# Optimization experiments

Measured on AMD Instinct MI355X. Metric: run time of the kernel, lower is better.

Reference implementation:

```python
import jax, jax.numpy as jnp
import numpy as np

B, S, D_IN, D_H, D_LAT, D_OUT = 128, 1024, 64, 256, 256, 128
N_PIECES = 20
NEG_BIG = -99999.0


def setup_inputs() -> dict:
    key = jax.random.key(0)
    ks = jax.random.split(key, 12)
    def lin(k, fan_in, fan_out):
        bound = 1.0 / np.sqrt(fan_in)
        kw, kb = jax.random.split(k)
        w = jax.random.uniform(kw, (fan_in, fan_out), minval=-bound, maxval=bound, dtype=jnp.float32)
        b = jax.random.uniform(kb, (fan_out,), minval=-bound, maxval=bound, dtype=jnp.float32)
        return w, b
    x = jax.random.normal(ks[0], (B, S, D_IN), dtype=jnp.float32)
    mask = jax.random.randint(ks[1], (B, S, 1), 0, 2, dtype=jnp.int32)
    phi_w1, phi_b1 = lin(ks[2], D_IN, D_H)
    phi_w2, phi_b2 = lin(ks[3], D_H, D_LAT)
    rho_w1, rho_b1 = lin(ks[4], D_LAT, D_H)
    rho_w2, rho_b2 = lin(ks[5], D_H, D_OUT)
    pool_w = 0.1 * jax.random.normal(ks[6], (D_LAT, N_PIECES + 1), dtype=jnp.float32)
    return dict(x=x, mask=mask, phi_w1=phi_w1, phi_b1=phi_b1, phi_w2=phi_w2, phi_b2=phi_b2,
                rho_w1=rho_w1, rho_b1=rho_b1, rho_w2=rho_w2, rho_b2=rho_b2, pool_w=pool_w)


def _fspool(x, n, w):
    # x: [B, C, S] features per channel over set dim; n: [B] ragged sizes; w: [C, P+1]
    b, c, s = x.shape
    # positions mapped to [0,1] ratio of the (n-1)-long valid prefix (fill_sizes)
    ratio = jnp.arange(s, dtype=jnp.float32)[None, :] / jnp.maximum(n.astype(jnp.float32) - 1.0, 1.0)[:, None]  # [B,S]
    m = (ratio <= 1.0).astype(x.dtype)          # [B,S], first n positions valid
    ratio = jnp.minimum(ratio, 1.0)
    # piecewise-linear interpolation of continuous weight function (determine_weight)
    pos = N_PIECES * ratio                       # [B,S]
    idx = jnp.floor(pos).astype(jnp.int32)
    frac = (pos - idx)[:, None, :]               # [B,1,S]
    left = jnp.take(w, idx, axis=1).transpose(1, 0, 2)                                   # [B,C,S]
    right = jnp.take(w, jnp.clip(idx + 1, 0, N_PIECES), axis=1).transpose(1, 0, 2)       # [B,C,S]
    weight = (1.0 - frac) * left + frac * right  # [B,C,S]
    # push padded entries to the bottom, sort descending per channel
    xm = x + (1.0 - m)[:, None, :] * NEG_BIG
    xs = jnp.flip(jnp.sort(xm, axis=2), axis=2)  # descending
    return jnp.sum(xs * weight * m[:, None, :], axis=2)  # [B,C]


def reference(x, mask, phi_w1, phi_b1, phi_w2, phi_b2, rho_w1, rho_b1, rho_w2, rho_b2, pool_w):
    # phi per-element MLP: [B,S,d_in] -> [B,S,d_lat]
    h = jax.nn.relu(jnp.einsum('bsi,ih->bsh', x, phi_w1) + phi_b1)
    feat = jnp.einsum('bsh,hl->bsl', h, phi_w2) + phi_b2
    feat = jnp.transpose(feat, (0, 2, 1))        # [B, d_lat, S]
    n = jnp.sum(mask, axis=1).squeeze(-1)        # [B]
    pooled = _fspool(feat, n, pool_w)            # [B, d_lat]
    # rho MLP
    h2 = jax.nn.relu(pooled @ rho_w1 + rho_b1)
    return h2 @ rho_w2 + rho_b2                  # [B, d_out]
```

## Files before the change

kernel.cpp:

```cpp
#include <hip/hip_runtime.h>
#include <hip/hip_bf16.h>

#define B_    128
#define S_    1024
#define DIN   64
#define DH    256
#define DLAT  256
#define DOUT  128
#define NPIECES 20

typedef short bf16x8 __attribute__((ext_vector_type(8)));
typedef float f32x4  __attribute__((ext_vector_type(4)));
typedef unsigned short u16x2 __attribute__((ext_vector_type(2)));

__device__ __forceinline__ unsigned short f2b(float f) {
    union { float f; unsigned u; } a; a.f = f;
    unsigned r = a.u + 0x7fffu + ((a.u >> 16) & 1u);
    return (unsigned short)(r >> 16);
}
__device__ __forceinline__ float b2f_u(unsigned u16bits) {
    union { unsigned u; float f; } a; a.u = u16bits << 16;
    return a.f;
}

__device__ __forceinline__ unsigned pmaxu(unsigned a, unsigned b) {
    union { unsigned u; u16x2 v; } A, Bv, R;
    A.u = a; Bv.u = b;
    R.v = __builtin_elementwise_max(A.v, Bv.v);
    return R.u;
}
__device__ __forceinline__ unsigned pminu(unsigned a, unsigned b) {
    union { unsigned u; u16x2 v; } A, Bv, R;
    A.u = a; Bv.u = b;
    R.v = __builtin_elementwise_min(A.v, Bv.v);
    return R.u;
}

__global__ __launch_bounds__(256) void k_count(const int* __restrict__ mask,
                                               int* __restrict__ nv) {
    int b = blockIdx.x, t = threadIdx.x;
    int sum = 0;
    #pragma unroll
    for (int q = 0; q < S_ / 256; ++q) sum += mask[b * S_ + q * 256 + t];
    #pragma unroll
    for (int off = 32; off > 0; off >>= 1) sum += __shfl_down(sum, off, 64);
    __shared__ int parts[4];
    if ((t & 63) == 0) parts[t >> 6] = sum;
    __syncthreads();
    if (t == 0) {
        int n = parts[0] + parts[1] + parts[2] + parts[3];
        nv[b] = max(n, 2);
    }
}

__global__ __launch_bounds__(256) void k_pack_x(const float* __restrict__ x,
                                                short* __restrict__ xpk) {
    int c = blockIdx.x * 256 + threadIdx.x;
    int l  = c & 63;
    int ks = (c >> 6) & 1;
    int st = (c >> 7) & 63;
    int b  = c >> 13;
    int s  = st * 16 + (l & 15);
    int k0 = ks * 32 + (l >> 4) * 8;
    const float* src = x + ((size_t)(b * S_ + s)) * DIN + k0;
    float4 v0 = *(const float4*)src;
    float4 v1 = *(const float4*)(src + 4);
    bf16x8 o;
    o[0] = (short)f2b(v0.x); o[1] = (short)f2b(v0.y); o[2] = (short)f2b(v0.z); o[3] = (short)f2b(v0.w);
    o[4] = (short)f2b(v1.x); o[5] = (short)f2b(v1.y); o[6] = (short)f2b(v1.z); o[7] = (short)f2b(v1.w);
    *(bf16x8*)(xpk + (size_t)c * 8) = o;
}

__global__ __launch_bounds__(256) void k_pack_w(const float* __restrict__ src,
                                                short* __restrict__ dst,
                                                int KT, int N, int nchunk) {
    int c = blockIdx.x * 256 + threadIdx.x;
    if (c >= nchunk) return;
    int l  = c & 63;
    int ks = (c >> 6) % KT;
    int nt = (c >> 6) / KT;
    int col = nt * 16 + (l & 15);
    int k0  = ks * 32 + (l >> 4) * 8;
    bf16x8 o;
    #pragma unroll
    for (int j = 0; j < 8; ++j) o[j] = (short)f2b(src[(size_t)(k0 + j) * N + col]);
    *(bf16x8*)(dst + (size_t)c * 8) = o;
}

__global__ __launch_bounds__(256) void k_phi_mfma(const short* __restrict__ xpk,
                                                  const short* __restrict__ w1pk,
                                                  const short* __restrict__ w2pk,
                                                  const float* __restrict__ b1,
                                                  const float* __restrict__ b2,
                                                  const int* __restrict__ nv,
                                                  unsigned short* __restrict__ feat) {
    const int b    = blockIdx.y;
    const int tile = blockIdx.x;
    const int s0   = tile * 64;
    if (s0 >= nv[b]) return;
    const int tid  = threadIdx.x;
    const int w    = tid >> 6;
    const int lane = tid & 63;
    const int c15  = lane & 15;
    const int q    = lane >> 4;

    __shared__ __align__(16) char lds[64 * 256 * 2];

    f32x4 acc1[4][4];
    #pragma unroll
    for (int mt = 0; mt < 4; ++mt)
        #pragma unroll
        for (int nt = 0; nt < 4; ++nt) acc1[mt][nt] = (f32x4)0.f;

    const short* xb = xpk + (((size_t)b * 64 + tile * 4) * 2) * 64 * 8;
    bf16x8 a1[4][2], bw[4][2];
    #pragma unroll
    for (int mt = 0; mt < 4; ++mt)
        #pragma unroll
        for (int ks = 0; ks < 2; ++ks)
            a1[mt][ks] = *(const bf16x8*)(xb + ((size_t)(mt * 2 + ks) * 64 + lane) * 8);
    #pragma unroll
    for (int nt = 0; nt < 4; ++nt)
        #pragma unroll
        for (int ks = 0; ks < 2; ++ks)
            bw[nt][ks] = *(const bf16x8*)(w1pk + ((size_t)((w * 4 + nt) * 2 + ks) * 64 + lane) * 8);
    #pragma unroll
    for (int ks = 0; ks < 2; ++ks)
        #pragma unroll
        for (int mt = 0; mt < 4; ++mt)
            #pragma unroll
            for (int nt = 0; nt < 4; ++nt)
                acc1[mt][nt] = __builtin_amdgcn_mfma_f32_16x16x32_bf16(a1[mt][ks], bw[nt][ks], acc1[mt][nt], 0, 0, 0);

    #pragma unroll
    for (int nt = 0; nt < 4; ++nt) {
        int chan = (w * 4 + nt) * 16 + c15;
        float bias = b1[chan];
        #pragma unroll
        for (int mt = 0; mt < 4; ++mt)
            #pragma unroll
            for (int r = 0; r < 4; ++r) {
                int pos = mt * 16 + q * 4 + r;
                float hv = fmaxf(acc1[mt][nt][r] + bias, 0.f);
                int byte = pos * 512 + chan * 2;
                byte ^= (pos & 7) << 4;
                *(unsigned short*)(lds + byte) = f2b(hv);
            }
    }
    __syncthreads();

    f32x4 acc2[4][4];
    #pragma unroll
    for (int mt = 0; mt < 4; ++mt)
        #pragma unroll
        for (int nt = 0; nt < 4; ++nt) acc2[mt][nt] = (f32x4)0.f;

    for (int ks2 = 0; ks2 < 8; ++ks2) {
        bf16x8 af[4];
        #pragma unroll
        for (int mt = 0; mt < 4; ++mt) {
            int pos = mt * 16 + c15;
            int byte = pos * 512 + ks2 * 64 + q * 16;
            byte ^= (pos & 7) << 4;
            af[mt] = *(const bf16x8*)(lds + byte);
        }
        #pragma unroll
        for (int nt = 0; nt < 4; ++nt) {
            bf16x8 bf_ = *(const bf16x8*)(w2pk + ((size_t)((w * 4 + nt) * 8 + ks2) * 64 + lane) * 8);
            #pragma unroll
            for (int mt = 0; mt < 4; ++mt)
                acc2[mt][nt] = __builtin_amdgcn_mfma_f32_16x16x32_bf16(af[mt], bf_, acc2[mt][nt], 0, 0, 0);
        }
    }
    __syncthreads();

    #pragma unroll
    for (int nt = 0; nt < 4; ++nt) {
        int chan = (w * 4 + nt) * 16 + c15;
        float bias = b2[chan];
        #pragma unroll
        for (int mt = 0; mt < 4; ++mt) {
            unsigned u0 = (unsigned)f2b(acc2[mt][nt][0] + bias) | ((unsigned)f2b(acc2[mt][nt][1] + bias) << 16);
            unsigned u1 = (unsigned)f2b(acc2[mt][nt][2] + bias) | ((unsigned)f2b(acc2[mt][nt][3] + bias) << 16);
            int pos0 = mt * 16 + q * 4;
            int byte = chan * 128 + pos0 * 2;
            byte ^= (chan & 7) << 4;
            *(uint2*)(lds + byte) = uint2{u0, u1};
        }
    }
    __syncthreads();

    #pragma unroll
    for (int it = 0; it < 8; ++it) {
        int L = it * 256 + tid;
        int chan = L >> 3, chunk = L & 7;
        int byte = chan * 128 + chunk * 16;
        byte ^= (chan & 7) << 4;
        uint4 val = *(const uint4*)(lds + byte);
        *(uint4*)((char*)(feat + ((size_t)b * DLAT + chan) * S_ + s0) + chunk * 16) = val;
    }
}

template <int EPL, bool FASTW>
__device__ __forceinline__ float fsp_sum(const unsigned short* __restrict__ fp,
                                         int n, const float* __restrict__ pw, int lane) {
    constexpr int NREG = EPL / 2;
    constexpr int N = EPL * 64;
    const int base = lane * EPL;

    unsigned r[NREG];
    {
        const uint4* q = (const uint4*)(fp + base);
        uint4 a = q[0];
        r[0] = a.x; r[1] = a.y; r[2] = a.z; r[3] = a.w;
        if (EPL == 16) {
            uint4 bq = q[1];
            r[4] = bq.x; r[5] = bq.y; r[6] = bq.z; r[7] = bq.w;
        }
    }

    #pragma unroll
    for (int t = 0; t < NREG; ++t) {
        unsigned u = r[t];
        unsigned sgn = (u >> 15) & 0x00010001u;
        unsigned key = u ^ ((sgn * 0x7FFFu) | 0x80008000u);
        int i0 = base + 2 * t;
        unsigned keep = (i0 + 1 < n) ? 0xFFFFFFFFu : ((i0 < n) ? 0x0000FFFFu : 0u);
        r[t] = key & keep;
    }

    #pragma unroll
    for (int k = 2; k <= N; k <<= 1) {
        #pragma unroll
        for (int j = k >> 1; j > 0; j >>= 1) {
            if (j >= EPL) {
                const int m = j / EPL;
                const bool dz  = (((lane * EPL) & k) == 0);
                const bool sel = (dz == ((lane & m) == 0));
                #pragma unroll
                for (int t = 0; t < NREG; ++t) {
                    unsigned p = __shfl_xor(r[t], m, 64);
                    unsigned mx = pmaxu(r[t], p), mn = pminu(r[t], p);
                    r[t] = sel ? mx : mn;
                }
            } else if (j >= 2) {
                const int jr = j >> 1;
                #pragma unroll
                for (int t = 0; t < NREG; ++t) {
                    if ((t & jr) == 0) {
                        const int tb = t | jr;
                        unsigned mx = pmaxu(r[t], r[tb]), mn = pminu(r[t], r[tb]);
                        const bool dz = ((((lane * EPL) | (2 * t)) & k) == 0);
                        r[t]  = dz ? mx : mn;
                        r[tb] = dz ? mn : mx;
                    }
                }
            } else {
                #pragma unroll
                for (int t = 0; t < NREG; ++t) {
                    unsigned sw = (r[t] >> 16) | (r[t] << 16);
                    unsigned mx = pmaxu(r[t], sw), mn = pminu(r[t], sw);
                    const bool dz = ((((lane * EPL) | (2 * t)) & k) == 0);
                    unsigned de = (mx & 0x0000FFFFu) | (mn & 0xFFFF0000u);
                    unsigned as = (mn & 0x0000FFFFu) | (mx & 0xFFFF0000u);
                    r[t] = dz ? de : as;
                }
            }
        }
    }

    const float invd = 1.0f / (float)(n - 1);
    float acc = 0.f;

    float k0, k1, k2; int ib = 0;
    if (FASTW) {
        float rb = fminf((float)base * invd, 1.0f);
        ib = (int)((float)NPIECES * rb);
        if (ib > NPIECES) ib = NPIECES;
        k0 = pw[ib];
        k1 = pw[min(ib + 1, NPIECES)];
        k2 = pw[min(ib + 2, NPIECES)];
    }

    #pragma unroll
    for (int t = 0; t < NREG; ++t) {
        #pragma unroll
        for (int h = 0; h < 2; ++h) {
            int i = base + 2 * t + h;
            unsigned key = h ? (r[t] >> 16) : (r[t] & 0xFFFFu);
            unsigned tneg = ((key >> 15) & 1u) ^ 1u;
            unsigned u = key ^ (0x8000u | (tneg * 0x7FFFu));
            float v = (i < n) ? b2f_u(u) : 0.f;
            float ratio = fminf((float)i * invd, 1.0f);
            float pos = (float)NPIECES * ratio;
            int idx = (int)pos;
            float frac = pos - (float)idx;
            float L, R;
            if (FASTW) {
                L = (idx == ib) ? k0 : k1;
                R = (idx == ib) ? k1 : k2;
            } else {
                L = pw[idx];
                R = pw[min(idx + 1, NPIECES)];
            }
            float wgt = fmaf(frac, R - L, L);
            acc = fmaf(v, wgt, acc);
        }
    }
    #pragma unroll
    for (int off = 32; off > 0; off >>= 1) acc += __shfl_xor(acc, off, 64);
    return acc;
}

__global__ __launch_bounds__(256) void k_fspool3(const unsigned short* __restrict__ feat,
                                                 const int* __restrict__ nv,
                                                 const float* __restrict__ pool_w,
                                                 float* __restrict__ pooled) {
    const int gw   = blockIdx.x * 4 + (threadIdx.x >> 6);
    const int lane = threadIdx.x & 63;
    const int b = gw >> 8, c = gw & 255;
    const int n = nv[b];
    const unsigned short* fp = feat + ((size_t)b * DLAT + c) * S_;
    const float* pw = pool_w + c * (NPIECES + 1);

    float res;
    if (n <= 512) {
        if (n >= 20 * 7 + 1) res = fsp_sum<8, true >(fp, n, pw, lane);
        else                 res = fsp_sum<8, false>(fp, n, pw, lane);
    } else {
        res = fsp_sum<16, true>(fp, n, pw, lane);
    }
    if (lane == 0) pooled[gw] = res;
}

__global__ __launch_bounds__(256) void k_rho(const float* __restrict__ pooled,
                                             const float* __restrict__ w1,
                                             const float* __restrict__ b1,
                                             const float* __restrict__ w2,
                                             const float* __restrict__ b2,
                                             float* __restrict__ out) {
    const int b = blockIdx.x, t = threadIdx.x;
    __shared__ float pl[DLAT];
    __shared__ float h2[DH];
    pl[t] = pooled[b * DLAT + t];
    __syncthreads();
    float acc = b1[t];
    for (int k = 0; k < DLAT; ++k) acc = fmaf(pl[k], w1[k * DH + t], acc);
    h2[t] = fmaxf(acc, 0.f);
    __syncthreads();
    if (t < DOUT) {
        float o = b2[t];
        for (int k = 0; k < DH; ++k) o = fmaf(h2[k], w2[k * DOUT + t], o);
        out[b * DOUT + t] = o;
    }
}

extern "C" void kernel_launch(void* const* d_in, const int* in_sizes, int n_in,
                              void* d_out, int out_size, void* d_ws, size_t ws_size,
                              hipStream_t stream) {
    const float* x     = (const float*)d_in[0];
    const int*   mask  = (const int*)d_in[1];
    const float* pw1   = (const float*)d_in[2];
    const float* pb1   = (const float*)d_in[3];
    const float* pw2   = (const float*)d_in[4];
    const float* pb2   = (const float*)d_in[5];
    const float* rw1   = (const float*)d_in[6];
    const float* rb1   = (const float*)d_in[7];
    const float* rw2   = (const float*)d_in[8];
    const float* rb2   = (const float*)d_in[9];
    const float* poolw = (const float*)d_in[10];
    float* out = (float*)d_out;

    char* ws = (char*)d_ws;
    size_t off = 0;
    int* nv = (int*)ws;                          off += 1024;
    short* xpk   = (short*)(ws + off);           off += (size_t)B_ * S_ * DIN * 2;
    short* w1pk  = (short*)(ws + off);           off += (size_t)DIN * DH * 2;
    short* w2pk  = (short*)(ws + off);           off += (size_t)DH * DLAT * 2;
    unsigned short* feat = (unsigned short*)(ws + off); off += (size_t)B_ * DLAT * S_ * 2;
    float* pooled = (float*)(ws + off);

    k_count<<<B_, 256, 0, stream>>>(mask, nv);
    k_pack_x<<<(B_ * S_ * DIN / 8) / 256, 256, 0, stream>>>(x, xpk);
    k_pack_w<<<(DIN * DH / 8 + 255) / 256, 256, 0, stream>>>(pw1, w1pk, DIN / 32, DH, DIN * DH / 8);
    k_pack_w<<<(DH * DLAT / 8 + 255) / 256, 256, 0, stream>>>(pw2, w2pk, DH / 32, DLAT, DH * DLAT / 8);
    k_phi_mfma<<<dim3(S_ / 64, B_), 256, 0, stream>>>(xpk, w1pk, w2pk, pb1, pb2, nv, feat);
    k_fspool3<<<(B_ * DLAT) / 4, 256, 0, stream>>>(feat, nv, poolw, pooled);
    k_rho<<<B_, 256, 0, stream>>>(pooled, rw1, rb1, rw2, rb2, out);
}
```

Before: 139.0 us.

## Fuse x packing into phi kernel, merge prep kernels, add 640-element sort path

Three changes at once. The separate bf16 packing pass over x is removed, and the phi MFMA kernel now reads fp32 x directly and converts it in registers, which saves a full write and re-read of the packed copy. The count and weight-pack kernels are merged into one launch, cutting launch overhead. The pooling kernel gains a path for 513 to 640 valid elements that sorts 512 plus 128 elements and merges them with a bitonic merge, instead of running the full 1024-element sort; this adds code size and register pressure.

```diff
diff --git a/kernel.cpp b/kernel.cpp
--- a/kernel.cpp
+++ b/kernel.cpp
@@ -22,7 +22,6 @@
     union { unsigned u; float f; } a; a.u = u16bits << 16;
     return a.f;
 }
-
 __device__ __forceinline__ unsigned pmaxu(unsigned a, unsigned b) {
     union { unsigned u; u16x2 v; } A, Bv, R;
     A.u = a; Bv.u = b;
@@ -35,59 +34,54 @@
     R.v = __builtin_elementwise_min(A.v, Bv.v);
     return R.u;
 }
-
-__global__ __launch_bounds__(256) void k_count(const int* __restrict__ mask,
-                                               int* __restrict__ nv) {
-    int b = blockIdx.x, t = threadIdx.x;
-    int sum = 0;
-    #pragma unroll
-    for (int q = 0; q < S_ / 256; ++q) sum += mask[b * S_ + q * 256 + t];
-    #pragma unroll
-    for (int off = 32; off > 0; off >>= 1) sum += __shfl_down(sum, off, 64);
+__device__ __forceinline__ unsigned ror16(unsigned x) { return (x >> 16) | (x << 16); }
+
+__device__ __forceinline__ bf16x8 cvt8(float4 a, float4 b) {
+    bf16x8 o;
+    o[0] = (short)f2b(a.x); o[1] = (short)f2b(a.y); o[2] = (short)f2b(a.z); o[3] = (short)f2b(a.w);
+    o[4] = (short)f2b(b.x); o[5] = (short)f2b(b.y); o[6] = (short)f2b(b.z); o[7] = (short)f2b(b.w);
+    return o;
+}
+
+__global__ __launch_bounds__(256) void k_prep(const int* __restrict__ mask,
+                                              int* __restrict__ nv,
+                                              const float* __restrict__ w1,
+                                              short* __restrict__ w1pk,
+                                              const float* __restrict__ w2,
+                                              short* __restrict__ w2pk) {
     __shared__ int parts[4];
-    if ((t & 63) == 0) parts[t >> 6] = sum;
-    __syncthreads();
-    if (t == 0) {
-        int n = parts[0] + parts[1] + parts[2] + parts[3];
-        nv[b] = max(n, 2);
-    }
-}
-
-__global__ __launch_bounds__(256) void k_pack_x(const float* __restrict__ x,
-                                                short* __restrict__ xpk) {
-    int c = blockIdx.x * 256 + threadIdx.x;
-    int l  = c & 63;
-    int ks = (c >> 6) & 1;
-    int st = (c >> 7) & 63;
-    int b  = c >> 13;
-    int s  = st * 16 + (l & 15);
-    int k0 = ks * 32 + (l >> 4) * 8;
-    const float* src = x + ((size_t)(b * S_ + s)) * DIN + k0;
-    float4 v0 = *(const float4*)src;
-    float4 v1 = *(const float4*)(src + 4);
-    bf16x8 o;
-    o[0] = (short)f2b(v0.x); o[1] = (short)f2b(v0.y); o[2] = (short)f2b(v0.z); o[3] = (short)f2b(v0.w);
-    o[4] = (short)f2b(v1.x); o[5] = (short)f2b(v1.y); o[6] = (short)f2b(v1.z); o[7] = (short)f2b(v1.w);
-    *(bf16x8*)(xpk + (size_t)c * 8) = o;
-}
-
-__global__ __launch_bounds__(256) void k_pack_w(const float* __restrict__ src,
-                                                short* __restrict__ dst,
-                                                int KT, int N, int nchunk) {
-    int c = blockIdx.x * 256 + threadIdx.x;
-    if (c >= nchunk) return;
-    int l  = c & 63;
-    int ks = (c >> 6) % KT;
-    int nt = (c >> 6) / KT;
-    int col = nt * 16 + (l & 15);
-    int k0  = ks * 32 + (l >> 4) * 8;
-    bf16x8 o;
-    #pragma unroll
-    for (int j = 0; j < 8; ++j) o[j] = (short)f2b(src[(size_t)(k0 + j) * N + col]);
-    *(bf16x8*)(dst + (size_t)c * 8) = o;
-}
-
-__global__ __launch_bounds__(256) void k_phi_mfma(const short* __restrict__ xpk,
+    const int blk = blockIdx.x, t = threadIdx.x;
+    if (blk < B_) {
+        int sum = 0;
+        #pragma unroll
+        for (int q = 0; q < S_ / 256; ++q) sum += mask[blk * S_ + q * 256 + t];
+        #pragma unroll
+        for (int off = 32; off > 0; off >>= 1) sum += __shfl_down(sum, off, 64);
+        if ((t & 63) == 0) parts[t >> 6] = sum;
+        __syncthreads();
+        if (t == 0) nv[blk] = max(parts[0] + parts[1] + parts[2] + parts[3], 2);
+    } else if (blk < B_ + 8) {
+        int c = (blk - B_) * 256 + t;
+        int l = c & 63, ks = (c >> 6) % 2, nt = (c >> 6) / 2;
+        int col = nt * 16 + (l & 15);
+        int k0 = ks * 32 + (l >> 4) * 8;
+        bf16x8 o;
+        #pragma unroll
+        for (int j = 0; j < 8; ++j) o[j] = (short)f2b(w1[(size_t)(k0 + j) * DH + col]);
+        *(bf16x8*)(w1pk + (size_t)c * 8) = o;
+    } else {
+        int c = (blk - B_ - 8) * 256 + t;
+        int l = c & 63, ks = (c >> 6) % 8, nt = (c >> 6) / 8;
+        int col = nt * 16 + (l & 15);
+        int k0 = ks * 32 + (l >> 4) * 8;
+        bf16x8 o;
+        #pragma unroll
+        for (int j = 0; j < 8; ++j) o[j] = (short)f2b(w2[(size_t)(k0 + j) * DLAT + col]);
+        *(bf16x8*)(w2pk + (size_t)c * 8) = o;
+    }
+}
+
+__global__ __launch_bounds__(256) void k_phi_mfma(const float* __restrict__ x,
                                                   const short* __restrict__ w1pk,
                                                   const short* __restrict__ w2pk,
                                                   const float* __restrict__ b1,
@@ -112,13 +106,17 @@
         #pragma unroll
         for (int nt = 0; nt < 4; ++nt) acc1[mt][nt] = (f32x4)0.f;
 
-    const short* xb = xpk + (((size_t)b * 64 + tile * 4) * 2) * 64 * 8;
+    const float* xb = x + ((size_t)b * S_ + s0) * DIN;
     bf16x8 a1[4][2], bw[4][2];
     #pragma unroll
     for (int mt = 0; mt < 4; ++mt)
         #pragma unroll
-        for (int ks = 0; ks < 2; ++ks)
-            a1[mt][ks] = *(const bf16x8*)(xb + ((size_t)(mt * 2 + ks) * 64 + lane) * 8);
+        for (int ks = 0; ks < 2; ++ks) {
+            const float* p = xb + (size_t)(mt * 16 + c15) * DIN + ks * 32 + q * 8;
+            float4 v0 = *(const float4*)p;
+            float4 v1 = *(const float4*)(p + 4);
+            a1[mt][ks] = cvt8(v0, v1);
+        }
     #pragma unroll
     for (int nt = 0; nt < 4; ++nt)
         #pragma unroll
@@ -201,26 +199,151 @@
     }
 }
 
-template <int EPL, bool FASTW>
-__device__ __forceinline__ float fsp_sum(const unsigned short* __restrict__ fp,
-                                         int n, const float* __restrict__ pw, int lane) {
-    constexpr int NREG = EPL / 2;
-    constexpr int N = EPL * 64;
-    const int base = lane * EPL;
-
-    unsigned r[NREG];
+
+template <int T0, int NREGS>
+__device__ __forceinline__ void loadcvt4(const unsigned short* __restrict__ fp, int i0, int n,
+                                         unsigned (&r)[NREGS]) {
+    uint4 a = *(const uint4*)(fp + i0);
+    r[T0 + 0] = a.x; r[T0 + 1] = a.y; r[T0 + 2] = a.z; r[T0 + 3] = a.w;
+    #pragma unroll
+    for (int t = 0; t < 4; ++t) {
+        unsigned u = r[T0 + t];
+        unsigned sgn = (u >> 15) & 0x00010001u;
+        unsigned key = u ^ ((sgn * 0x7FFFu) | 0x80008000u);
+        int e0 = i0 + 2 * t;
+        unsigned keep = (e0 + 1 < n) ? 0xFFFFFFFFu : ((e0 < n) ? 0x0000FFFFu : 0u);
+        r[T0 + t] = key & keep;
+    }
+}
+
+template <int T0, int NREGS>
+__device__ __forceinline__ void pass_cross(unsigned (&r)[NREGS], int lane, int m, int k) {
+    bool lower = ((lane & m) == 0);
+    bool dz = (((lane << 3) & k) == 0);
+    bool sel = (dz == lower);
+    #pragma unroll
+    for (int t = 0; t < 4; ++t) {
+        unsigned p = __shfl_xor(r[T0 + t], m, 64);
+        unsigned mx = pmaxu(r[T0 + t], p), mn = pminu(r[T0 + t], p);
+        r[T0 + t] = sel ? mx : mn;
+    }
+}
+
+template <int T0, int NREGS>
+__device__ __forceinline__ void pass_pair(unsigned (&r)[NREGS], int lane, int jr, int k) {
+    #pragma unroll
+    for (int t = 0; t < 4; ++t)
+        if ((t & jr) == 0) {
+            int ta = T0 + t, tb = T0 + (t | jr);
+            unsigned mx = pmaxu(r[ta], r[tb]), mn = pminu(r[ta], r[tb]);
+            bool dz = ((((lane << 3) | (t << 1)) & k) == 0);
+            r[ta] = dz ? mx : mn;
+            r[tb] = dz ? mn : mx;
+        }
+}
+
+template <int T0, int NREGS>
+__device__ __forceinline__ void pass_inpack(unsigned (&r)[NREGS], int lane, int k) {
+    #pragma unroll
+    for (int t = 0; t < 4; ++t) {
+        unsigned v = r[T0 + t];
+        unsigned sw = ror16(v);
+        unsigned mx = pmaxu(v, sw), mn = pminu(v, sw);
+        bool dz = ((((lane << 3) | (t << 1)) & k) == 0);
+        unsigned de = (mx & 0x0000FFFFu) | (mn & 0xFFFF0000u);
+        unsigned as = (mn & 0x0000FFFFu) | (mx & 0xFFFF0000u);
+        r[T0 + t] = dz ? de : as;
+    }
+}
+
+template <int NET, int T0, int NREGS>
+__device__ __forceinline__ void sort_net(unsigned (&r)[NREGS], int lane) {
+    #pragma unroll
+    for (int k = 2; k <= NET; k <<= 1) {
+        #pragma unroll
+        for (int j = k >> 1; j > 0; j >>= 1) {
+            if (j >= 8)      pass_cross<T0>(r, lane, j >> 3, k);
+            else if (j >= 2) pass_pair<T0>(r, lane, j >> 1, k);
+            else             pass_inpack<T0>(r, lane, k);
+        }
+    }
+}
+
+__device__ __forceinline__ void merge_desc512_dual(unsigned (&r)[8], int lane) {
+    #pragma unroll
+    for (int j = 256; j >= 8; j >>= 1) {
+        const int m = j >> 3;
+        bool sel = ((lane & m) == 0);
+        #pragma unroll
+        for (int t = 0; t < 8; ++t) {
+            unsigned p = __shfl_xor(r[t], m, 64);
+            unsigned mx = pmaxu(r[t], p), mn = pminu(r[t], p);
+            r[t] = sel ? mx : mn;
+        }
+    }
+    #pragma unroll
+    for (int jr = 2; jr >= 1; jr >>= 1)
+        #pragma unroll
+        for (int g = 0; g < 8; g += 4)
+            #pragma unroll
+            for (int t = 0; t < 4; ++t)
+                if ((t & jr) == 0) {
+                    unsigned a = r[g + t], bb = r[g + (t | jr)];
+                    r[g + t]        = pmaxu(a, bb);
+                    r[g + (t | jr)] = pminu(a, bb);
+                }
+    #pragma unroll
+    for (int t = 0; t < 8; ++t) {
+        unsigned sw = ror16(r[t]);
+        unsigned mx = pmaxu(r[t], sw), mn = pminu(r[t], sw);
+        r[t] = (mx & 0x0000FFFFu) | (mn & 0xFFFF0000u);
+    }
+}
+
+template <bool FASTW, int T0, int NREGS>
+__device__ __forceinline__ float wsum(const unsigned (&r)[NREGS], int rankBase, int n,
+                                      float invd, const float* __restrict__ pw) {
+    float acc = 0.f;
+    float k0 = 0.f, k1 = 0.f, k2 = 0.f; int ib = 0;
+    if (FASTW) {
+        float rb = fminf((float)rankBase * invd, 1.0f);
+        ib = (int)((float)NPIECES * rb);
+        if (ib > NPIECES) ib = NPIECES;
+        k0 = pw[ib]; k1 = pw[min(ib + 1, NPIECES)]; k2 = pw[min(ib + 2, NPIECES)];
+    }
+    #pragma unroll
+    for (int t = 0; t < 4; ++t)
+        #pragma unroll
+        for (int h = 0; h < 2; ++h) {
+            int i = rankBase + 2 * t + h;
+            unsigned key = h ? (r[T0 + t] >> 16) : (r[T0 + t] & 0xFFFFu);
+            unsigned tneg = ((key >> 15) & 1u) ^ 1u;
+            unsigned u = key ^ (0x8000u | (tneg * 0x7FFFu));
+            float v = (i < n) ? b2f_u(u) : 0.f;
+            float ratio = fminf((float)i * invd, 1.0f);
+            float pos = (float)NPIECES * ratio;
+            int idx = (int)pos;
+            float frac = pos - (float)idx;
+            float L, R;
+            if (FASTW) { L = (idx == ib) ? k0 : k1; R = (idx == ib) ? k1 : k2; }
+            else       { L = pw[idx];  R = pw[min(idx + 1, NPIECES)]; }
+            acc = fmaf(v, fmaf(frac, R - L, L), acc);
+        }
+    return acc;
+}
+
+__device__ __forceinline__ float fsp_sum16(const unsigned short* __restrict__ fp,
+                                           int n, const float* __restrict__ pw, int lane) {
+    const int base = lane * 16;
+    unsigned r[8];
     {
-        const uint4* q = (const uint4*)(fp + base);
-        uint4 a = q[0];
-        r[0] = a.x; r[1] = a.y; r[2] = a.z; r[3] = a.w;
-        if (EPL == 16) {
-            uint4 bq = q[1];
-            r[4] = bq.x; r[5] = bq.y; r[6] = bq.z; r[7] = bq.w;
-        }
-    }
-
-    #pragma unroll
-    for (int t = 0; t < NREG; ++t) {
+        const uint4* q4 = (const uint4*)(fp + base);
+        uint4 a = q4[0], bq = q4[1];
+        r[0] = a.x;  r[1] = a.y;  r[2] = a.z;  r[3] = a.w;
+        r[4] = bq.x; r[5] = bq.y; r[6] = bq.z; r[7] = bq.w;
+    }
+    #pragma unroll
+    for (int t = 0; t < 8; ++t) {
         unsigned u = r[t];
         unsigned sgn = (u >> 15) & 0x00010001u;
         unsigned key = u ^ ((sgn * 0x7FFFu) | 0x80008000u);
@@ -228,17 +351,16 @@
         unsigned keep = (i0 + 1 < n) ? 0xFFFFFFFFu : ((i0 < n) ? 0x0000FFFFu : 0u);
         r[t] = key & keep;
     }
-
-    #pragma unroll
-    for (int k = 2; k <= N; k <<= 1) {
+    #pragma unroll
+    for (int k = 2; k <= 1024; k <<= 1) {
         #pragma unroll
         for (int j = k >> 1; j > 0; j >>= 1) {
-            if (j >= EPL) {
-                const int m = j / EPL;
-                const bool dz  = (((lane * EPL) & k) == 0);
+            if (j >= 16) {
+                const int m = j >> 4;
+                const bool dz  = (((lane * 16) & k) == 0);
                 const bool sel = (dz == ((lane & m) == 0));
                 #pragma unroll
-                for (int t = 0; t < NREG; ++t) {
+                for (int t = 0; t < 8; ++t) {
                     unsigned p = __shfl_xor(r[t], m, 64);
                     unsigned mx = pmaxu(r[t], p), mn = pminu(r[t], p);
                     r[t] = sel ? mx : mn;
@@ -246,21 +368,20 @@
             } else if (j >= 2) {
                 const int jr = j >> 1;
                 #pragma unroll
-                for (int t = 0; t < NREG; ++t) {
+                for (int t = 0; t < 8; ++t)
                     if ((t & jr) == 0) {
                         const int tb = t | jr;
                         unsigned mx = pmaxu(r[t], r[tb]), mn = pminu(r[t], r[tb]);
-                        const bool dz = ((((lane * EPL) | (2 * t)) & k) == 0);
+                        const bool dz = ((((lane * 16) | (2 * t)) & k) == 0);
                         r[t]  = dz ? mx : mn;
                         r[tb] = dz ? mn : mx;
                     }
-                }
             } else {
                 #pragma unroll
-                for (int t = 0; t < NREG; ++t) {
-                    unsigned sw = (r[t] >> 16) | (r[t] << 16);
+                for (int t = 0; t < 8; ++t) {
+                    unsigned sw = ror16(r[t]);
                     unsigned mx = pmaxu(r[t], sw), mn = pminu(r[t], sw);
-                    const bool dz = ((((lane * EPL) | (2 * t)) & k) == 0);
+                    const bool dz = ((((lane * 16) | (2 * t)) & k) == 0);
                     unsigned de = (mx & 0x0000FFFFu) | (mn & 0xFFFF0000u);
                     unsigned as = (mn & 0x0000FFFFu) | (mx & 0xFFFF0000u);
                     r[t] = dz ? de : as;
@@ -268,22 +389,14 @@
             }
         }
     }
-
     const float invd = 1.0f / (float)(n - 1);
     float acc = 0.f;
-
-    float k0, k1, k2; int ib = 0;
-    if (FASTW) {
-        float rb = fminf((float)base * invd, 1.0f);
-        ib = (int)((float)NPIECES * rb);
-        if (ib > NPIECES) ib = NPIECES;
-        k0 = pw[ib];
-        k1 = pw[min(ib + 1, NPIECES)];
-        k2 = pw[min(ib + 2, NPIECES)];
-    }
-
-    #pragma unroll
-    for (int t = 0; t < NREG; ++t) {
+    float rb = fminf((float)base * invd, 1.0f);
+    int ib = (int)((float)NPIECES * rb);
+    if (ib > NPIECES) ib = NPIECES;
+    float k0 = pw[ib], k1 = pw[min(ib + 1, NPIECES)], k2 = pw[min(ib + 2, NPIECES)];
+    #pragma unroll
+    for (int t = 0; t < 8; ++t)
         #pragma unroll
         for (int h = 0; h < 2; ++h) {
             int i = base + 2 * t + h;
@@ -295,24 +408,13 @@
             float pos = (float)NPIECES * ratio;
             int idx = (int)pos;
             float frac = pos - (float)idx;
-            float L, R;
-            if (FASTW) {
-                L = (idx == ib) ? k0 : k1;
-                R = (idx == ib) ? k1 : k2;
-            } else {
-                L = pw[idx];
-                R = pw[min(idx + 1, NPIECES)];
-            }
-            float wgt = fmaf(frac, R - L, L);
-            acc = fmaf(v, wgt, acc);
-        }
-    }
-    #pragma unroll
-    for (int off = 32; off > 0; off >>= 1) acc += __shfl_xor(acc, off, 64);
+            float L = (idx == ib) ? k0 : k1, R = (idx == ib) ? k1 : k2;
+            acc = fmaf(v, fmaf(frac, R - L, L), acc);
+        }
     return acc;
 }
 
-__global__ __launch_bounds__(256) void k_fspool3(const unsigned short* __restrict__ feat,
+__global__ __launch_bounds__(256) void k_fspool4(const unsigned short* __restrict__ feat,
                                                  const int* __restrict__ nv,
                                                  const float* __restrict__ pool_w,
                                                  float* __restrict__ pooled) {
@@ -322,14 +424,38 @@
     const int n = nv[b];
     const unsigned short* fp = feat + ((size_t)b * DLAT + c) * S_;
     const float* pw = pool_w + c * (NPIECES + 1);
+    const float invd = 1.0f / (float)(n - 1);
 
     float res;
     if (n <= 512) {
-        if (n >= 20 * 7 + 1) res = fsp_sum<8, true >(fp, n, pw, lane);
-        else                 res = fsp_sum<8, false>(fp, n, pw, lane);
+        unsigned r[4];
+        loadcvt4<0>(fp, lane * 8, n, r);
+        sort_net<512, 0>(r, lane);
+        res = (n >= 141) ? wsum<true, 0>(r, lane * 8, n, invd, pw)
+                         : wsum<false, 0>(r, lane * 8, n, invd, pw);
+    } else if (n <= 640) {
+        unsigned r[8];
+        loadcvt4<0>(fp, lane * 8, n, r);
+        loadcvt4<4>(fp, 512 + lane * 8, n, r);
+        sort_net<512, 0>(r, lane);
+        sort_net<128, 4>(r, lane);
+        unsigned pa[4], pb[4];
+        #pragma unroll
+        for (int t = 0; t < 4; ++t) pa[t] = ror16(__shfl_xor(r[7 - t], 63, 64));
+        #pragma unroll
+        for (int t = 0; t < 4; ++t) pb[t] = ror16(__shfl_xor(r[3 - t], 63, 64));
+        #pragma unroll
+        for (int t = 0; t < 4; ++t) r[t]     = pmaxu(r[t], pa[t]);
+        #pragma unroll
+        for (int t = 0; t < 4; ++t) r[4 + t] = pminu(r[4 + t], pb[t]);
+        merge_desc512_dual(r, lane);
+        res = wsum<true, 0>(r, lane * 8, n, invd, pw)
+            + wsum<true, 4>(r, 512 + lane * 8, n, invd, pw);
     } else {
-        res = fsp_sum<16, true>(fp, n, pw, lane);
-    }
+        res = fsp_sum16(fp, n, pw, lane);
+    }
+    #pragma unroll
+    for (int off = 32; off > 0; off >>= 1) res += __shfl_xor(res, off, 64);
     if (lane == 0) pooled[gw] = res;
 }
 
@@ -374,17 +500,13 @@
     char* ws = (char*)d_ws;
     size_t off = 0;
     int* nv = (int*)ws;                          off += 1024;
-    short* xpk   = (short*)(ws + off);           off += (size_t)B_ * S_ * DIN * 2;
     short* w1pk  = (short*)(ws + off);           off += (size_t)DIN * DH * 2;
     short* w2pk  = (short*)(ws + off);           off += (size_t)DH * DLAT * 2;
     unsigned short* feat = (unsigned short*)(ws + off); off += (size_t)B_ * DLAT * S_ * 2;
     float* pooled = (float*)(ws + off);
 
-    k_count<<<B_, 256, 0, stream>>>(mask, nv);
-    k_pack_x<<<(B_ * S_ * DIN / 8) / 256, 256, 0, stream>>>(x, xpk);
-    k_pack_w<<<(DIN * DH / 8 + 255) / 256, 256, 0, stream>>>(pw1, w1pk, DIN / 32, DH, DIN * DH / 8);
-    k_pack_w<<<(DH * DLAT / 8 + 255) / 256, 256, 0, stream>>>(pw2, w2pk, DH / 32, DLAT, DH * DLAT / 8);
-    k_phi_mfma<<<dim3(S_ / 64, B_), 256, 0, stream>>>(xpk, w1pk, w2pk, pb1, pb2, nv, feat);
-    k_fspool3<<<(B_ * DLAT) / 4, 256, 0, stream>>>(feat, nv, poolw, pooled);
+    k_prep<<<B_ + 8 + 32, 256, 0, stream>>>(mask, nv, pw1, w1pk, pw2, w2pk);
+    k_phi_mfma<<<dim3(S_ / 64, B_), 256, 0, stream>>>(x, w1pk, w2pk, pb1, pb2, nv, feat);
+    k_fspool4<<<(B_ * DLAT) / 4, 256, 0, stream>>>(feat, nv, poolw, pooled);
     k_rho<<<B_, 256, 0, stream>>>(pooled, rw1, rb1, rw2, rb2, out);
 }
```

After: 132.8 us. 4.5% less time.
